# Performance work log

Hardware: AMD Instinct MI355X
Metric: run time of the kernel (lower is better)

Reference implementation:

```python
import jax, jax.numpy as jnp
import numpy as np

B, T, D = 64, 512, 512
H, DH = 8, 64  # head_num, att_embedding_size; H*DH == D
NEG = jnp.float32(-2.0**32 + 1)


def _pos_encoding(t, d):
    # Position_Embedding (mode='sum'): [cos, sin] concat over d/2 frequencies
    inv_freq = 1.0 / jnp.power(10000.0, 2.0 * jnp.arange(d // 2, dtype=jnp.float32) / d)
    pij = jnp.arange(t, dtype=jnp.float32)[:, None] * inv_freq[None, :]  # (T, d/2)
    return jnp.concatenate([jnp.cos(pij), jnp.sin(pij)], axis=-1)  # (T, d)


def setup_inputs() -> dict:
    key = jax.random.key(0)
    ks = jax.random.split(key, 9)
    queries = jax.random.normal(ks[0], (B, T, D), dtype=jnp.float32)
    keys = jax.random.normal(ks[1], (B, T, D), dtype=jnp.float32)
    query_lens = jax.random.randint(ks[2], (B, 1), 1, T + 1)
    key_lens = jax.random.randint(ks[3], (B, 1), 1, T + 1)
    W_Q = jax.random.truncated_normal(ks[4], -2., 2., (D, H * DH), dtype=jnp.float32) * 0.05
    W_K = jax.random.truncated_normal(ks[5], -2., 2., (D, H * DH), dtype=jnp.float32) * 0.05
    W_V = jax.random.truncated_normal(ks[6], -2., 2., (D, H * DH), dtype=jnp.float32) * 0.05
    fw1 = jax.random.normal(ks[7], (H * DH, 4 * H * DH), dtype=jnp.float32) * 0.02
    fw2 = jax.random.normal(ks[8], (4 * H * DH, H * DH), dtype=jnp.float32) * 0.02
    return {"queries": queries, "keys": keys, "query_lens": query_lens,
            "key_lens": key_lens, "W_Q": W_Q, "W_K": W_K, "W_V": W_V,
            "fw1": fw1, "fw2": fw2}


def reference(queries, keys, query_lens, key_lens, W_Q, W_K, W_V, fw1, fw2):
    # sequence masks (B, T) from lengths (B, 1)
    ar = jnp.arange(T)
    q_mask = (ar[None, :] < query_lens).astype(jnp.float32)  # (B, T)
    k_mask = ar[None, :] < key_lens                          # (B, T) bool

    pe = _pos_encoding(T, D)[None]  # (1, T, D)
    q_in = queries + pe
    k_in = keys + pe

    qp = jnp.einsum('btd,de->bte', q_in, W_Q).reshape(B, T, H, DH)
    kp = jnp.einsum('btd,de->bte', k_in, W_K)
    # DeepCTR quirk: values projected from the already-projected keys
    vp = jnp.einsum('btd,de->bte', kp, W_V).reshape(B, T, H, DH)
    kp = kp.reshape(B, T, H, DH)

    scores = jnp.einsum('bthd,bshd->bhts', qp, kp) / jnp.sqrt(jnp.float32(DH))
    scores = jnp.where(k_mask[:, None, None, :], scores, NEG)
    scores = scores - jnp.max(scores, axis=-1, keepdims=True)
    attn = jax.nn.softmax(scores, axis=-1)
    attn = attn * q_mask[:, None, :, None]

    out = jnp.einsum('bhts,bshd->bthd', attn, vp).reshape(B, T, H * DH)
    result = out + q_in  # residual uses PE-augmented queries

    ff = jnp.einsum('btd,df->btf', jax.nn.relu(jnp.einsum('btd,df->btf', result, fw1)), fw2)
    result = result + ff

    return jnp.mean(result, axis=1, keepdims=True)  # (B, 1, D)
```

## Files before the change

kernel.cpp:

```cpp
#include <hip/hip_runtime.h>

typedef unsigned short u16;
typedef __attribute__((ext_vector_type(8))) short short8;
typedef __attribute__((ext_vector_type(4))) float floatx4;

#define QSCALE 0.1803368801111204f

__device__ __forceinline__ u16 f2bf(float x) {
  union { float f; unsigned u; } un; un.f = x;
  unsigned r = un.u + 0x7fffu + ((un.u >> 16) & 1u);
  return (u16)(r >> 16);
}
__device__ __forceinline__ float bf2f(u16 h) {
  union { unsigned u; float f; } un; un.u = ((unsigned)h) << 16;
  return un.f;
}
__device__ __forceinline__ void gld16(const u16* g, u16* l) {
  __builtin_amdgcn_global_load_lds((__attribute__((address_space(1))) void*)g,
                                   (__attribute__((address_space(3))) void*)l, 16, 0, 0);
}

__global__ __launch_bounds__(256) void wtrans_all(const float* __restrict__ W_Q,
                                                  const float* __restrict__ W_K,
                                                  const float* __restrict__ fw1,
                                                  u16* __restrict__ WqT, u16* __restrict__ WkT,
                                                  u16* __restrict__ F1T) {
  __shared__ float tile[32][33];
  int L = blockIdx.x;
  const float* in;
  u16* out;
  int N, bx, by;
  if (L < 256) { in = W_Q; out = WqT; N = 512; bx = L & 15; by = L >> 4; }
  else if (L < 512) { L -= 256; in = W_K; out = WkT; N = 512; bx = L & 15; by = L >> 4; }
  else { L -= 512; in = fw1; out = F1T; N = 2048; bx = L & 63; by = L >> 6; }
  int tx = threadIdx.x, ty = threadIdx.y;
  int n0 = bx * 32, k0 = by * 32;
#pragma unroll
  for (int i = 0; i < 4; i++) {
    int kk = ty + i * 8;
    tile[kk][tx] = in[(size_t)(k0 + kk) * N + n0 + tx];
  }
  __syncthreads();
#pragma unroll
  for (int i = 0; i < 4; i++) {
    int nn = ty + i * 8;
    out[(size_t)(n0 + nn) * 512 + k0 + tx] = f2bf(tile[tx][nn]);
  }
}

__global__ __launch_bounds__(256) void wkv_kernel(const float* __restrict__ WK,
                                                  const float* __restrict__ WV,
                                                  u16* __restrict__ WkvT) {
  __shared__ float Kt[32][36];
  __shared__ float Vt[32][36];
  int nt = blockIdx.x & 15, dt = blockIdx.x >> 4;
  int n0 = nt * 32, d0 = dt * 32;
  int tid = threadIdx.x;
  int flat = tid * 4;
  int i4 = flat >> 5, j4 = flat & 31;
  int tn = tid & 15, td = tid >> 4;
  float acc00 = 0.f, acc01 = 0.f, acc10 = 0.f, acc11 = 0.f;
  for (int e0 = 0; e0 < 512; e0 += 32) {
    __syncthreads();
    *(float4*)&Kt[i4][j4] = *(const float4*)&WK[(size_t)(d0 + i4) * 512 + e0 + j4];
    *(float4*)&Vt[i4][j4] = *(const float4*)&WV[(size_t)(e0 + i4) * 512 + n0 + j4];
    __syncthreads();
#pragma unroll 8
    for (int e = 0; e < 32; e++) {
      float k0v = Kt[td * 2][e], k1v = Kt[td * 2 + 1][e];
      float v0 = Vt[e][tn * 2], v1 = Vt[e][tn * 2 + 1];
      acc00 += k0v * v0; acc01 += k0v * v1;
      acc10 += k1v * v0; acc11 += k1v * v1;
    }
  }
  size_t o = (size_t)(n0 + tn * 2) * 512 + d0 + td * 2;
  WkvT[o] = f2bf(acc00);
  WkvT[o + 1] = f2bf(acc10);
  WkvT[o + 512] = f2bf(acc01);
  WkvT[o + 513] = f2bf(acc11);
}

__global__ __launch_bounds__(256) void pe_add_kernel(const float* __restrict__ q,
                                                     const float* __restrict__ k,
                                                     u16* __restrict__ qb, u16* __restrict__ kb) {
  size_t flat = ((size_t)blockIdx.x * 256 + threadIdx.x) * 4;
  int d0 = (int)(flat & 511);
  int t = (int)((flat >> 9) & 511);
  const float4 qv = *(const float4*)(q + flat);
  const float4 kv = *(const float4*)(k + flat);
  float pe[4];
#pragma unroll
  for (int i = 0; i < 4; i++) {
    int d = d0 + i;
    int j = (d < 256) ? d : d - 256;
    float f = exp2f((float)j * -0.05190512648f);
    float arg = (float)t * f;
    pe[i] = (d < 256) ? cosf(arg) : sinf(arg);
  }
  u16 qo[4], ko[4];
  qo[0] = f2bf(qv.x + pe[0]); qo[1] = f2bf(qv.y + pe[1]);
  qo[2] = f2bf(qv.z + pe[2]); qo[3] = f2bf(qv.w + pe[3]);
  ko[0] = f2bf(kv.x + pe[0]); ko[1] = f2bf(kv.y + pe[1]);
  ko[2] = f2bf(kv.z + pe[2]); ko[3] = f2bf(kv.w + pe[3]);
  *(uint2*)(qb + flat) = *(const uint2*)qo;
  *(uint2*)(kb + flat) = *(const uint2*)ko;
}

template <int EPI, int MODE>
__global__ __launch_bounds__(256) void gemm_bt(const u16* __restrict__ A, const u16* __restrict__ Bt,
                                               u16* __restrict__ C, int NX, int KS, int N, int K,
                                               float* __restrict__ outp,
                                               const u16* __restrict__ A2, const u16* __restrict__ Bt2,
                                               u16* __restrict__ C2,
                                               const u16* __restrict__ A3, const u16* __restrict__ Bt3,
                                               u16* __restrict__ C3) {
  __shared__ u16 pool[16640];
  u16* Alds = pool;
  u16* Blds = pool + 8192;
  const int tid = threadIdx.x;
  const int lane = tid & 63, w = tid >> 6;
  const int quad = lane >> 4, cl = lane & 15;
  const int wm = w >> 1, wn = w & 1;
  int L = blockIdx.x;
  int seg = 0;
  if (MODE == 2) {
    int third = gridDim.x / 3;
    seg = L / third;
    L -= seg * third;
    if (seg == 1) { A = A2; Bt = Bt2; C = C2; }
    else if (seg == 2) { A = A3; Bt = Bt3; C = C3; }
  }
  const int xcd = L & 7, s = L >> 3;
  const int nx = s % NX;
  const int t2 = s / NX;
  const int ksl = t2 % KS;
  const int rgrp = t2 / KS;
  const int tm = (rgrp * 8 + xcd) * 128;
  const int tn = nx * 128;
  const int kbase = ksl * (K / KS);
  floatx4 acc[4][4] = {};
  const int nk = (K / KS) >> 6;
  const int srow = lane >> 3;
  const int sg = (lane & 7) ^ srow;
  for (int ks = 0; ks < nk; ks++) {
    __syncthreads();
    const int k0 = kbase + (ks << 6);
#pragma unroll
    for (int i = 0; i < 4; i++) {
      int c = w * 4 + i;
      int row = c * 8 + srow;
      gld16(A + ((size_t)(tm + row) * K + k0 + sg * 8), &Alds[c * 512]);
      gld16(Bt + ((size_t)(tn + row) * K + k0 + sg * 8), &Blds[c * 512]);
    }
    __syncthreads();
#pragma unroll
    for (int kh = 0; kh < 2; kh++) {
      short8 af[4], bfr[4];
      const int ga = (((kh << 2) + quad) ^ (cl & 7)) * 8;
#pragma unroll
      for (int f = 0; f < 4; f++) {
        af[f] = *(const short8*)&Alds[(wm * 64 + f * 16 + cl) * 64 + ga];
        bfr[f] = *(const short8*)&Blds[(wn * 64 + f * 16 + cl) * 64 + ga];
      }
#pragma unroll
      for (int fm = 0; fm < 4; fm++)
#pragma unroll
        for (int fn = 0; fn < 4; fn++)
          acc[fm][fn] = __builtin_amdgcn_mfma_f32_16x16x32_bf16(af[fm], bfr[fn], acc[fm][fn], 0, 0, 0);
    }
  }
  if constexpr (MODE == 2) {
    if (seg < 2) {
#pragma unroll
      for (int fm = 0; fm < 4; fm++)
#pragma unroll
        for (int fn = 0; fn < 4; fn++)
#pragma unroll
          for (int r = 0; r < 4; r++) {
            int row = tm + wm * 64 + fm * 16 + quad * 4 + r;
            int col = tn + wn * 64 + fn * 16 + cl;
            C[(size_t)row * N + col] = f2bf(acc[fm][fn][r]);
          }
    } else {
      __syncthreads();
      u16* Tr = pool;
#pragma unroll
      for (int fm = 0; fm < 4; fm++)
#pragma unroll
        for (int fn = 0; fn < 4; fn++)
#pragma unroll
          for (int r = 0; r < 4; r++) {
            int row = wm * 64 + fm * 16 + quad * 4 + r;
            int col = wn * 64 + fn * 16 + cl;
            Tr[col * 130 + row] = f2bf(acc[fm][fn][r]);
          }
      __syncthreads();
      int col = tid >> 1, half = tid & 1;
      int b = tm >> 9, gcol = tn + col;
      int h = gcol >> 6, d = gcol & 63;
      int s0 = (tm & 511) + half * 64;
      u16* dst = C + ((size_t)((b * 8 + h) * 64 + d) * 512 + s0);
      const u16* src = &Tr[col * 130 + half * 64];
#pragma unroll
      for (int j = 0; j < 8; j++) *(short8*)(dst + j * 8) = *(const short8*)(src + j * 8);
    }
  } else if constexpr (EPI == 0) {
#pragma unroll
    for (int fm = 0; fm < 4; fm++)
#pragma unroll
      for (int fn = 0; fn < 4; fn++)
#pragma unroll
        for (int r = 0; r < 4; r++) {
          int row = tm + wm * 64 + fm * 16 + quad * 4 + r;
          int col = tn + wn * 64 + fn * 16 + cl;
          C[(size_t)row * N + col] = f2bf(acc[fm][fn][r]);
        }
  }
}

__global__ __launch_bounds__(512, 2) void ffn1_256(const u16* __restrict__ A,
                                                   const u16* __restrict__ Bt,
                                                   float* __restrict__ outp) {
  __shared__ u16 lds[65536];
  const int K = 512;
  const int tid = threadIdx.x;
  const int lane = tid & 63, w = tid >> 6;
  const int quad = lane >> 4, cl = lane & 15;
  const int wm = w >> 2, wn = w & 3;
  int L = blockIdx.x;
  const int xcd = L & 7, s = L >> 3;
  const int nx = s & 7;
  const int rgrp = s >> 3;
  const int tm = (rgrp * 8 + xcd) * 256;
  const int tn = nx * 256;
  const int srow = lane >> 3;
  const int sg = (lane & 7) ^ srow;
  const int cb = w * 4;

  floatx4 acc[8][4] = {};

  {
    u16* Ab = lds;
    u16* Bb = lds + 16384;
#pragma unroll
    for (int i = 0; i < 4; i++) {
      int cc = cb + i, row = cc * 8 + srow;
      gld16(A + ((size_t)(tm + row) * K + sg * 8), &Ab[cc * 512]);
    }
#pragma unroll
    for (int i = 0; i < 4; i++) {
      int cc = cb + i, row = cc * 8 + srow;
      gld16(Bt + ((size_t)(tn + row) * K + sg * 8), &Bb[cc * 512]);
    }
  }

  const int nk = K >> 6;
#pragma unroll 1
  for (int kt = 0; kt < nk; kt++) {
    u16* Ab = lds + (kt & 1) * 32768;
    u16* Bb = Ab + 16384;
    u16* An = lds + ((kt & 1) ^ 1) * 32768;
    u16* Bn = An + 16384;
    const bool pf = (kt + 1 < nk);
    const int k0n = (kt + 1) << 6;
    if (pf) {
#pragma unroll
      for (int i = 0; i < 4; i++) {
        int cc = cb + i, row = cc * 8 + srow;
        gld16(A + ((size_t)(tm + row) * K + k0n + sg * 8), &An[cc * 512]);
      }
      asm volatile("s_waitcnt vmcnt(4)" ::: "memory");
    } else {
      asm volatile("s_waitcnt vmcnt(0)" ::: "memory");
    }
    __builtin_amdgcn_s_barrier();
    short8 a0[4][2], b0[2][2];
#pragma unroll
    for (int f = 0; f < 4; f++)
#pragma unroll
      for (int kh = 0; kh < 2; kh++)
        a0[f][kh] = *(const short8*)&Ab[(wm * 128 + f * 16 + cl) * 64 + ((((kh << 2) + quad)) ^ (cl & 7)) * 8];
#pragma unroll
    for (int n = 0; n < 2; n++)
#pragma unroll
      for (int kh = 0; kh < 2; kh++)
        b0[n][kh] = *(const short8*)&Bb[(wn * 64 + n * 16 + cl) * 64 + ((((kh << 2) + quad)) ^ (cl & 7)) * 8];
    __builtin_amdgcn_s_setprio(1);
#pragma unroll
    for (int f = 0; f < 4; f++)
#pragma unroll
      for (int n = 0; n < 2; n++)
#pragma unroll
        for (int kh = 0; kh < 2; kh++)
          acc[f][n] = __builtin_amdgcn_mfma_f32_16x16x32_bf16(a0[f][kh], b0[n][kh], acc[f][n], 0, 0, 0);
    __builtin_amdgcn_s_setprio(0);
    __builtin_amdgcn_s_barrier();
    if (pf) {
#pragma unroll
      for (int i = 0; i < 4; i++) {
        int cc = cb + i, row = cc * 8 + srow;
        gld16(Bt + ((size_t)(tn + row) * K + k0n + sg * 8), &Bn[cc * 512]);
      }
    }
    short8 b1[2][2];
#pragma unroll
    for (int n = 0; n < 2; n++)
#pragma unroll
      for (int kh = 0; kh < 2; kh++)
        b1[n][kh] = *(const short8*)&Bb[(wn * 64 + (n + 2) * 16 + cl) * 64 + ((((kh << 2) + quad)) ^ (cl & 7)) * 8];
    __builtin_amdgcn_s_setprio(1);
#pragma unroll
    for (int f = 0; f < 4; f++)
#pragma unroll
      for (int n = 0; n < 2; n++)
#pragma unroll
        for (int kh = 0; kh < 2; kh++)
          acc[f][n + 2] = __builtin_amdgcn_mfma_f32_16x16x32_bf16(a0[f][kh], b1[n][kh], acc[f][n + 2], 0, 0, 0);
    __builtin_amdgcn_s_setprio(0);
    __builtin_amdgcn_s_barrier();
    short8 a1[4][2];
#pragma unroll
    for (int f = 0; f < 4; f++)
#pragma unroll
      for (int kh = 0; kh < 2; kh++)
        a1[f][kh] = *(const short8*)&Ab[(wm * 128 + (f + 4) * 16 + cl) * 64 + ((((kh << 2) + quad)) ^ (cl & 7)) * 8];
    __builtin_amdgcn_s_setprio(1);
#pragma unroll
    for (int f = 0; f < 4; f++)
#pragma unroll
      for (int n = 0; n < 2; n++)
#pragma unroll
        for (int kh = 0; kh < 2; kh++)
          acc[f + 4][n + 2] = __builtin_amdgcn_mfma_f32_16x16x32_bf16(a1[f][kh], b1[n][kh], acc[f + 4][n + 2], 0, 0, 0);
    __builtin_amdgcn_s_setprio(0);
    __builtin_amdgcn_s_barrier();
    __builtin_amdgcn_s_setprio(1);
#pragma unroll
    for (int f = 0; f < 4; f++)
#pragma unroll
      for (int n = 0; n < 2; n++)
#pragma unroll
        for (int kh = 0; kh < 2; kh++)
          acc[f + 4][n] = __builtin_amdgcn_mfma_f32_16x16x32_bf16(a1[f][kh], b0[n][kh], acc[f + 4][n], 0, 0, 0);
    __builtin_amdgcn_s_setprio(0);
    __builtin_amdgcn_s_barrier();
  }

  float cs[4] = {0.f, 0.f, 0.f, 0.f};
#pragma unroll
  for (int f = 0; f < 8; f++)
#pragma unroll
    for (int n = 0; n < 4; n++)
#pragma unroll
      for (int r = 0; r < 4; r++) cs[n] += fmaxf(acc[f][n][r], 0.0f);
#pragma unroll
  for (int n = 0; n < 4; n++) {
    cs[n] += __shfl_xor(cs[n], 16);
    cs[n] += __shfl_xor(cs[n], 32);
  }
  if (quad == 0) {
    int b = tm >> 9;
#pragma unroll
    for (int n = 0; n < 4; n++)
      atomicAdd(outp + (size_t)b * 2048 + tn + wn * 64 + n * 16 + cl, cs[n]);
  }
}

__global__ __launch_bounds__(256) void ffn2_mean_kernel(const float* __restrict__ sums,
                                                        const float* __restrict__ fw2,
                                                        float* __restrict__ outp) {
  __shared__ float s[128];
  int fs = blockIdx.x & 15, b = blockIdx.x >> 4;
  int tid = threadIdx.x;
  if (tid < 128) s[tid] = sums[(size_t)b * 2048 + fs * 128 + tid];
  __syncthreads();
  const float* w = fw2 + (size_t)(fs * 128) * 512;
  float a0 = 0.f, a1 = 0.f;
#pragma unroll 4
  for (int f = 0; f < 128; f++) {
    float sv = s[f];
    a0 += sv * w[(size_t)f * 512 + tid];
    a1 += sv * w[(size_t)f * 512 + 256 + tid];
  }
  atomicAdd(outp + b * 512 + tid, a0 * (1.0f / 512.0f));
  atomicAdd(outp + b * 512 + 256 + tid, a1 * (1.0f / 512.0f));
}

__global__ __launch_bounds__(256) void attn_kernel(const u16* __restrict__ qp, const u16* __restrict__ kp,
                                                   const u16* __restrict__ vT, const u16* __restrict__ qin,
                                                   u16* __restrict__ resout, const int* __restrict__ qlen,
                                                   const int* __restrict__ klen, float* __restrict__ outp) {
  __shared__ u16 KPu[8704];
  __shared__ u16 Vlds[64 * 128];
  __shared__ float Csum[4][64];
  int L = blockIdx.x;
  int xcd = L & 7;
  int idx = L >> 3;
  int qt = idx & 7;
  int g = xcd + (idx >> 3) * 8;
  int h = g & 7, b = g >> 3;
  int tid = threadIdx.x, lane = tid & 63, w = tid >> 6;
  int quad = lane >> 4, cl = lane & 15;
  int kl = klen[b], ql = qlen[b];
  int q0 = qt * 64 + w * 16;

  if (qt * 64 >= ql) {
    int c = tid & 63, r0 = (tid >> 6) * 16;
    float sv = 0.f;
#pragma unroll
    for (int i = 0; i < 16; i++) {
      size_t idx2 = ((size_t)(b * 512 + qt * 64 + r0 + i) * 512) + h * 64 + c;
      u16 val = qin[idx2];
      resout[idx2] = val;
      sv += bf2f(val);
    }
    Csum[w][c] = sv;
    __syncthreads();
    if (tid < 64) {
      float t = Csum[0][tid] + Csum[1][tid] + Csum[2][tid] + Csum[3][tid];
      atomicAdd(outp + b * 512 + h * 64 + tid, t * (1.0f / 512.0f));
    }
    return;
  }
  bool wactive = q0 < ql;

  short8 qfrag[2];
#pragma unroll
  for (int ks = 0; ks < 2; ks++)
    qfrag[ks] = *(const short8*)(qp + ((size_t)(b * 512 + q0 + cl) * 512 + h * 64 + ks * 32 + quad * 8));
  const short8 ones8 = {(short)0x3F80, (short)0x3F80, (short)0x3F80, (short)0x3F80,
                        (short)0x3F80, (short)0x3F80, (short)0x3F80, (short)0x3F80};
  float m_r[4];
  floatx4 o[4] = {};
  floatx4 lacc = {};
#pragma unroll
  for (int r = 0; r < 4; r++) m_r[r] = -3.0e38f;

  int nkt = (kl + 127) >> 7;
  for (int kt = 0; kt < nkt; kt++) {
    __syncthreads();
#pragma unroll
    for (int i = 0; i < 4; i++) {
      int c = w * 4 + i;
      int row = c * 8 + (lane >> 3);
      int gc = (lane & 7) ^ (row & 7);
      gld16(kp + ((size_t)(b * 512 + kt * 128 + row) * 512 + h * 64 + gc * 8), &KPu[c * 512]);
    }
#pragma unroll
    for (int i = 0; i < 4; i++) {
      int c = w * 4 + i;
      int row = c * 4 + (lane >> 4);
      int gc = (lane & 15) ^ (row & 7);
      gld16(vT + ((size_t)((b * 8 + h) * 64 + row) * 512 + kt * 128 + gc * 8), &Vlds[c * 512]);
    }
    asm volatile("s_waitcnt vmcnt(4)" ::: "memory");
    __builtin_amdgcn_s_barrier();
    __builtin_amdgcn_sched_barrier(0);
    floatx4 sacc[8] = {};
    float mnew[4], alpha[4];
    if (wactive) {
      __builtin_amdgcn_s_setprio(1);
#pragma unroll
      for (int f = 0; f < 8; f++) {
        int krow = f * 16 + cl;
#pragma unroll
        for (int ks = 0; ks < 2; ks++) {
          int kc = ks * 4 + quad;
          short8 kf = *(const short8*)&KPu[krow * 64 + ((kc ^ (cl & 7)) * 8)];
          sacc[f] = __builtin_amdgcn_mfma_f32_16x16x32_bf16(qfrag[ks], kf, sacc[f], 0, 0, 0);
        }
      }
      __builtin_amdgcn_s_setprio(0);
#pragma unroll
      for (int r = 0; r < 4; r++) mnew[r] = m_r[r];
#pragma unroll
      for (int f = 0; f < 8; f++) {
        int key = kt * 128 + f * 16 + cl;
        bool ok = key < kl;
#pragma unroll
        for (int r = 0; r < 4; r++) {
          float v = ok ? sacc[f][r] * QSCALE : -4294967296.0f;
          sacc[f][r] = v;
          mnew[r] = fmaxf(mnew[r], v);
        }
      }
#pragma unroll
      for (int mk = 1; mk <= 8; mk <<= 1)
#pragma unroll
        for (int r = 0; r < 4; r++) mnew[r] = fmaxf(mnew[r], __shfl_xor(mnew[r], mk));
#pragma unroll
      for (int r = 0; r < 4; r++) {
        alpha[r] = exp2f(m_r[r] - mnew[r]);
        m_r[r] = mnew[r];
      }
    }
    __syncthreads();
    if (wactive) {
      u16* P = &KPu[w * 2176];
#pragma unroll
      for (int f = 0; f < 8; f++)
#pragma unroll
        for (int r = 0; r < 4; r++) {
          float p = exp2f(sacc[f][r] - mnew[r]);
          P[(quad * 4 + r) * 136 + f * 16 + cl] = f2bf(p);
        }
#pragma unroll
      for (int r = 0; r < 4; r++) lacc[r] *= alpha[r];
#pragma unroll
      for (int fd = 0; fd < 4; fd++)
#pragma unroll
        for (int r = 0; r < 4; r++) o[fd][r] *= alpha[r];
      __builtin_amdgcn_s_setprio(1);
#pragma unroll
      for (int k2 = 0; k2 < 4; k2++) {
        short8 pf = *(const short8*)&P[cl * 136 + k2 * 32 + quad * 8];
        lacc = __builtin_amdgcn_mfma_f32_16x16x32_bf16(pf, ones8, lacc, 0, 0, 0);
#pragma unroll
        for (int fd = 0; fd < 4; fd++) {
          int vrow = fd * 16 + cl;
          int sc = k2 * 4 + quad;
          short8 vf = *(const short8*)&Vlds[vrow * 128 + ((sc ^ (cl & 7)) * 8)];
          o[fd] = __builtin_amdgcn_mfma_f32_16x16x32_bf16(pf, vf, o[fd], 0, 0, 0);
        }
      }
      __builtin_amdgcn_s_setprio(0);
    }
  }
  float colsum[4] = {0.f, 0.f, 0.f, 0.f};
#pragma unroll
  for (int fd = 0; fd < 4; fd++)
#pragma unroll
    for (int r = 0; r < 4; r++) {
      int q = q0 + quad * 4 + r;
      float v = o[fd][r] / lacc[r];
      if (q >= ql) v = 0.f;
      size_t idx2 = (size_t)(b * 512 + q) * 512 + h * 64 + fd * 16 + cl;
      v += bf2f(qin[idx2]);
      resout[idx2] = f2bf(v);
      colsum[fd] += v;
    }
#pragma unroll
  for (int fd = 0; fd < 4; fd++) {
    colsum[fd] += __shfl_xor(colsum[fd], 16);
    colsum[fd] += __shfl_xor(colsum[fd], 32);
  }
  if (quad == 0) {
#pragma unroll
    for (int fd = 0; fd < 4; fd++) Csum[w][fd * 16 + cl] = colsum[fd];
  }
  __syncthreads();
  if (tid < 64) {
    float t = Csum[0][tid] + Csum[1][tid] + Csum[2][tid] + Csum[3][tid];
    atomicAdd(outp + b * 512 + h * 64 + tid, t * (1.0f / 512.0f));
  }
}

extern "C" void kernel_launch(void* const* d_in, const int* in_sizes, int n_in,
                              void* d_out, int out_size, void* d_ws, size_t ws_size,
                              hipStream_t stream) {
  const float* queries = (const float*)d_in[0];
  const float* keys = (const float*)d_in[1];
  const int* qlen = (const int*)d_in[2];
  const int* klen = (const int*)d_in[3];
  const float* W_Q = (const float*)d_in[4];
  const float* W_K = (const float*)d_in[5];
  const float* W_V = (const float*)d_in[6];
  const float* fw1 = (const float*)d_in[7];
  const float* fw2 = (const float*)d_in[8];
  float* outp = (float*)d_out;
  char* ws = (char*)d_ws;

  constexpr size_t SZ_W = 512 * 512 * 2;
  constexpr size_t SZ_F = 2048 * 512 * 2;
  constexpr size_t SZ_S = 64 * 2048 * 4;
  constexpr size_t SZ_T = (size_t)64 * 512 * 512 * 2;
  size_t o_WqT = 0;
  size_t o_WkT = o_WqT + SZ_W;
  size_t o_Wkv = o_WkT + SZ_W;
  size_t o_F1T = o_Wkv + SZ_W;
  size_t o_SUM = o_F1T + SZ_F;
  size_t o_ABCD = o_SUM + SZ_S;
  size_t o_E = o_ABCD + 4 * SZ_T;
  size_t NEED = o_E + SZ_T;
  if (ws_size < NEED) return;

  u16* WqT = (u16*)(ws + o_WqT);
  u16* WkT = (u16*)(ws + o_WkT);
  u16* WkvT = (u16*)(ws + o_Wkv);
  u16* F1T = (u16*)(ws + o_F1T);
  float* sums = (float*)(ws + o_SUM);
  u16* q_in = (u16*)(ws + o_ABCD);
  u16* k_in = (u16*)(ws + o_ABCD + SZ_T);
  u16* qp = (u16*)(ws + o_ABCD + 2 * SZ_T);
  u16* kpb = (u16*)(ws + o_ABCD + 3 * SZ_T);
  u16* vT = (u16*)(ws + o_E);
  u16* resb = k_in;

  hipMemsetAsync(d_out, 0, (size_t)out_size * sizeof(float), stream);
  hipMemsetAsync(sums, 0, SZ_S, stream);

  wtrans_all<<<1536, dim3(32, 8), 0, stream>>>(W_Q, W_K, fw1, WqT, WkT, F1T);
  wkv_kernel<<<256, 256, 0, stream>>>(W_K, W_V, WkvT);
  pe_add_kernel<<<16384, 256, 0, stream>>>(queries, keys, q_in, k_in);

  gemm_bt<0, 2><<<3 * 1024, 256, 0, stream>>>(q_in, WqT, qp, 4, 1, 512, 512, nullptr,
                                              k_in, WkT, kpb, k_in, WkvT, vT);

  attn_kernel<<<4096, 256, 0, stream>>>(qp, kpb, vT, q_in, resb, qlen, klen, outp);

  ffn1_256<<<1024, 512, 0, stream>>>(resb, F1T, sums);
  ffn2_mean_kernel<<<1024, 256, 0, stream>>>(sums, fw2, outp);
}
```

Baseline: 404.6 us.

## Use 256x256 double-buffered projection GEMM and precompute positional encoding table

Measured after the change: 397.9 us. About the same (-1.7%).

```diff
diff --git a/kernel.cpp b/kernel.cpp
--- a/kernel.cpp
+++ b/kernel.cpp
@@ -80,14 +80,10 @@
   WkvT[o + 513] = f2bf(acc11);
 }
 
-__global__ __launch_bounds__(256) void pe_add_kernel(const float* __restrict__ q,
-                                                     const float* __restrict__ k,
-                                                     u16* __restrict__ qb, u16* __restrict__ kb) {
-  size_t flat = ((size_t)blockIdx.x * 256 + threadIdx.x) * 4;
-  int d0 = (int)(flat & 511);
-  int t = (int)((flat >> 9) & 511);
-  const float4 qv = *(const float4*)(q + flat);
-  const float4 kv = *(const float4*)(k + flat);
+__global__ __launch_bounds__(256) void pe_table_kernel(float* __restrict__ pet) {
+  int flat = (blockIdx.x * 256 + threadIdx.x) * 4;
+  int d0 = flat & 511;
+  int t = flat >> 9;
   float pe[4];
 #pragma unroll
   for (int i = 0; i < 4; i++) {
@@ -97,124 +93,202 @@
     float arg = (float)t * f;
     pe[i] = (d < 256) ? cosf(arg) : sinf(arg);
   }
+  *(float4*)(pet + flat) = *(const float4*)pe;
+}
+
+__global__ __launch_bounds__(256) void pe_add_kernel(const float* __restrict__ q,
+                                                     const float* __restrict__ k,
+                                                     const float* __restrict__ pet,
+                                                     u16* __restrict__ qb, u16* __restrict__ kb) {
+  size_t flat = ((size_t)blockIdx.x * 256 + threadIdx.x) * 4;
+  const float4 qv = *(const float4*)(q + flat);
+  const float4 kv = *(const float4*)(k + flat);
+  const float4 pv = *(const float4*)(pet + (flat & 262143));
   u16 qo[4], ko[4];
-  qo[0] = f2bf(qv.x + pe[0]); qo[1] = f2bf(qv.y + pe[1]);
-  qo[2] = f2bf(qv.z + pe[2]); qo[3] = f2bf(qv.w + pe[3]);
-  ko[0] = f2bf(kv.x + pe[0]); ko[1] = f2bf(kv.y + pe[1]);
-  ko[2] = f2bf(kv.z + pe[2]); ko[3] = f2bf(kv.w + pe[3]);
+  qo[0] = f2bf(qv.x + pv.x); qo[1] = f2bf(qv.y + pv.y);
+  qo[2] = f2bf(qv.z + pv.z); qo[3] = f2bf(qv.w + pv.w);
+  ko[0] = f2bf(kv.x + pv.x); ko[1] = f2bf(kv.y + pv.y);
+  ko[2] = f2bf(kv.z + pv.z); ko[3] = f2bf(kv.w + pv.w);
   *(uint2*)(qb + flat) = *(const uint2*)qo;
   *(uint2*)(kb + flat) = *(const uint2*)ko;
 }
 
-template <int EPI, int MODE>
-__global__ __launch_bounds__(256) void gemm_bt(const u16* __restrict__ A, const u16* __restrict__ Bt,
-                                               u16* __restrict__ C, int NX, int KS, int N, int K,
-                                               float* __restrict__ outp,
-                                               const u16* __restrict__ A2, const u16* __restrict__ Bt2,
-                                               u16* __restrict__ C2,
-                                               const u16* __restrict__ A3, const u16* __restrict__ Bt3,
-                                               u16* __restrict__ C3) {
-  __shared__ u16 pool[16640];
-  u16* Alds = pool;
-  u16* Blds = pool + 8192;
+__global__ __launch_bounds__(512, 2) void proj_256(const u16* __restrict__ q_in,
+                                                   const u16* __restrict__ k_in,
+                                                   const u16* __restrict__ WqT,
+                                                   const u16* __restrict__ WkT,
+                                                   const u16* __restrict__ WkvT,
+                                                   u16* __restrict__ qp,
+                                                   u16* __restrict__ kpb,
+                                                   u16* __restrict__ vTp) {
+  __shared__ u16 lds[65536];
+  const int K = 512;
   const int tid = threadIdx.x;
   const int lane = tid & 63, w = tid >> 6;
   const int quad = lane >> 4, cl = lane & 15;
-  const int wm = w >> 1, wn = w & 1;
+  const int wm = w >> 2, wn = w & 3;
   int L = blockIdx.x;
-  int seg = 0;
-  if (MODE == 2) {
-    int third = gridDim.x / 3;
-    seg = L / third;
-    L -= seg * third;
-    if (seg == 1) { A = A2; Bt = Bt2; C = C2; }
-    else if (seg == 2) { A = A3; Bt = Bt3; C = C3; }
-  }
+  const int seg = L >> 8;
+  L &= 255;
+  const u16* A = (seg == 0) ? q_in : k_in;
+  const u16* Bt = (seg == 0) ? WqT : (seg == 1) ? WkT : WkvT;
   const int xcd = L & 7, s = L >> 3;
-  const int nx = s % NX;
-  const int t2 = s / NX;
-  const int ksl = t2 % KS;
-  const int rgrp = t2 / KS;
-  const int tm = (rgrp * 8 + xcd) * 128;
-  const int tn = nx * 128;
-  const int kbase = ksl * (K / KS);
-  floatx4 acc[4][4] = {};
-  const int nk = (K / KS) >> 6;
+  const int nx = s & 1;
+  const int rgrp = s >> 1;
+  const int tm = (rgrp * 8 + xcd) * 256;
+  const int tn = nx * 256;
   const int srow = lane >> 3;
   const int sg = (lane & 7) ^ srow;
-  for (int ks = 0; ks < nk; ks++) {
-    __syncthreads();
-    const int k0 = kbase + (ks << 6);
+  const int cb = w * 4;
+
+  floatx4 acc[8][4] = {};
+
+  {
+    u16* Ab = lds;
+    u16* Bb = lds + 16384;
 #pragma unroll
     for (int i = 0; i < 4; i++) {
-      int c = w * 4 + i;
-      int row = c * 8 + srow;
-      gld16(A + ((size_t)(tm + row) * K + k0 + sg * 8), &Alds[c * 512]);
-      gld16(Bt + ((size_t)(tn + row) * K + k0 + sg * 8), &Blds[c * 512]);
-    }
-    __syncthreads();
-#pragma unroll
-    for (int kh = 0; kh < 2; kh++) {
-      short8 af[4], bfr[4];
-      const int ga = (((kh << 2) + quad) ^ (cl & 7)) * 8;
-#pragma unroll
-      for (int f = 0; f < 4; f++) {
-        af[f] = *(const short8*)&Alds[(wm * 64 + f * 16 + cl) * 64 + ga];
-        bfr[f] = *(const short8*)&Blds[(wn * 64 + f * 16 + cl) * 64 + ga];
-      }
-#pragma unroll
-      for (int fm = 0; fm < 4; fm++)
-#pragma unroll
-        for (int fn = 0; fn < 4; fn++)
-          acc[fm][fn] = __builtin_amdgcn_mfma_f32_16x16x32_bf16(af[fm], bfr[fn], acc[fm][fn], 0, 0, 0);
-    }
-  }
-  if constexpr (MODE == 2) {
-    if (seg < 2) {
-#pragma unroll
-      for (int fm = 0; fm < 4; fm++)
-#pragma unroll
-        for (int fn = 0; fn < 4; fn++)
-#pragma unroll
-          for (int r = 0; r < 4; r++) {
-            int row = tm + wm * 64 + fm * 16 + quad * 4 + r;
-            int col = tn + wn * 64 + fn * 16 + cl;
-            C[(size_t)row * N + col] = f2bf(acc[fm][fn][r]);
-          }
+      int cc = cb + i, row = cc * 8 + srow;
+      gld16(A + ((size_t)(tm + row) * K + sg * 8), &Ab[cc * 512]);
+    }
+#pragma unroll
+    for (int i = 0; i < 4; i++) {
+      int cc = cb + i, row = cc * 8 + srow;
+      gld16(Bt + ((size_t)(tn + row) * K + sg * 8), &Bb[cc * 512]);
+    }
+  }
+
+  const int nk = K >> 6;
+#pragma unroll 1
+  for (int kt = 0; kt < nk; kt++) {
+    u16* Ab = lds + (kt & 1) * 32768;
+    u16* Bb = Ab + 16384;
+    u16* An = lds + ((kt & 1) ^ 1) * 32768;
+    u16* Bn = An + 16384;
+    const bool pf = (kt + 1 < nk);
+    const int k0n = (kt + 1) << 6;
+    if (pf) {
+#pragma unroll
+      for (int i = 0; i < 4; i++) {
+        int cc = cb + i, row = cc * 8 + srow;
+        gld16(A + ((size_t)(tm + row) * K + k0n + sg * 8), &An[cc * 512]);
+      }
+#pragma unroll
+      for (int i = 0; i < 4; i++) {
+        int cc = cb + i, row = cc * 8 + srow;
+        gld16(Bt + ((size_t)(tn + row) * K + k0n + sg * 8), &Bn[cc * 512]);
+      }
+      asm volatile("s_waitcnt vmcnt(8)" ::: "memory");
     } else {
+      asm volatile("s_waitcnt vmcnt(0)" ::: "memory");
+    }
+    __builtin_amdgcn_s_barrier();
+    short8 a0[4][2], b0[2][2];
+#pragma unroll
+    for (int f = 0; f < 4; f++)
+#pragma unroll
+      for (int kh = 0; kh < 2; kh++)
+        a0[f][kh] = *(const short8*)&Ab[(wm * 128 + f * 16 + cl) * 64 + ((((kh << 2) + quad)) ^ (cl & 7)) * 8];
+#pragma unroll
+    for (int n = 0; n < 2; n++)
+#pragma unroll
+      for (int kh = 0; kh < 2; kh++)
+        b0[n][kh] = *(const short8*)&Bb[(wn * 64 + n * 16 + cl) * 64 + ((((kh << 2) + quad)) ^ (cl & 7)) * 8];
+    __builtin_amdgcn_s_setprio(1);
+#pragma unroll
+    for (int f = 0; f < 4; f++)
+#pragma unroll
+      for (int n = 0; n < 2; n++)
+#pragma unroll
+        for (int kh = 0; kh < 2; kh++)
+          acc[f][n] = __builtin_amdgcn_mfma_f32_16x16x32_bf16(a0[f][kh], b0[n][kh], acc[f][n], 0, 0, 0);
+    __builtin_amdgcn_s_setprio(0);
+    __builtin_amdgcn_s_barrier();
+    short8 b1[2][2];
+#pragma unroll
+    for (int n = 0; n < 2; n++)
+#pragma unroll
+      for (int kh = 0; kh < 2; kh++)
+        b1[n][kh] = *(const short8*)&Bb[(wn * 64 + (n + 2) * 16 + cl) * 64 + ((((kh << 2) + quad)) ^ (cl & 7)) * 8];
+    __builtin_amdgcn_s_setprio(1);
+#pragma unroll
+    for (int f = 0; f < 4; f++)
+#pragma unroll
+      for (int n = 0; n < 2; n++)
+#pragma unroll
+        for (int kh = 0; kh < 2; kh++)
+          acc[f][n + 2] = __builtin_amdgcn_mfma_f32_16x16x32_bf16(a0[f][kh], b1[n][kh], acc[f][n + 2], 0, 0, 0);
+    __builtin_amdgcn_s_setprio(0);
+    __builtin_amdgcn_s_barrier();
+    short8 a1[4][2];
+#pragma unroll
+    for (int f = 0; f < 4; f++)
+#pragma unroll
+      for (int kh = 0; kh < 2; kh++)
+        a1[f][kh] = *(const short8*)&Ab[(wm * 128 + (f + 4) * 16 + cl) * 64 + ((((kh << 2) + quad)) ^ (cl & 7)) * 8];
+    __builtin_amdgcn_s_setprio(1);
+#pragma unroll
+    for (int f = 0; f < 4; f++)
+#pragma unroll
+      for (int n = 0; n < 2; n++)
+#pragma unroll
+        for (int kh = 0; kh < 2; kh++)
+          acc[f + 4][n + 2] = __builtin_amdgcn_mfma_f32_16x16x32_bf16(a1[f][kh], b1[n][kh], acc[f + 4][n + 2], 0, 0, 0);
+    __builtin_amdgcn_s_setprio(0);
+    __builtin_amdgcn_s_barrier();
+    __builtin_amdgcn_s_setprio(1);
+#pragma unroll
+    for (int f = 0; f < 4; f++)
+#pragma unroll
+      for (int n = 0; n < 2; n++)
+#pragma unroll
+        for (int kh = 0; kh < 2; kh++)
+          acc[f + 4][n] = __builtin_amdgcn_mfma_f32_16x16x32_bf16(a1[f][kh], b0[n][kh], acc[f + 4][n], 0, 0, 0);
+    __builtin_amdgcn_s_setprio(0);
+    __builtin_amdgcn_s_barrier();
+  }
+
+  if (seg < 2) {
+    u16* C = (seg == 0) ? qp : kpb;
+#pragma unroll
+    for (int f = 0; f < 8; f++)
+#pragma unroll
+      for (int n = 0; n < 4; n++)
+#pragma unroll
+        for (int r = 0; r < 4; r++) {
+          int row = tm + wm * 128 + f * 16 + quad * 4 + r;
+          int col = tn + wn * 64 + n * 16 + cl;
+          C[(size_t)row * 512 + col] = f2bf(acc[f][n][r]);
+        }
+  } else {
+    const int b = tm >> 9, sbase = tm & 511;
+#pragma unroll 1
+    for (int p = 0; p < 2; p++) {
       __syncthreads();
-      u16* Tr = pool;
-#pragma unroll
-      for (int fm = 0; fm < 4; fm++)
-#pragma unroll
-        for (int fn = 0; fn < 4; fn++)
-#pragma unroll
-          for (int r = 0; r < 4; r++) {
-            int row = wm * 64 + fm * 16 + quad * 4 + r;
-            int col = wn * 64 + fn * 16 + cl;
-            Tr[col * 130 + row] = f2bf(acc[fm][fn][r]);
-          }
+      if ((wn >> 1) == p) {
+        int cbase = (wn & 1) * 64;
+#pragma unroll
+        for (int f = 0; f < 8; f++)
+#pragma unroll
+          for (int n = 0; n < 4; n++)
+#pragma unroll
+            for (int r = 0; r < 4; r++) {
+              int tc = cbase + n * 16 + cl;
+              int row = wm * 128 + f * 16 + quad * 4 + r;
+              lds[tc * 264 + row] = f2bf(acc[f][n][r]);
+            }
+      }
       __syncthreads();
-      int col = tid >> 1, half = tid & 1;
-      int b = tm >> 9, gcol = tn + col;
-      int h = gcol >> 6, d = gcol & 63;
-      int s0 = (tm & 511) + half * 64;
-      u16* dst = C + ((size_t)((b * 8 + h) * 64 + d) * 512 + s0);
-      const u16* src = &Tr[col * 130 + half * 64];
-#pragma unroll
-      for (int j = 0; j < 8; j++) *(short8*)(dst + j * 8) = *(const short8*)(src + j * 8);
-    }
-  } else if constexpr (EPI == 0) {
-#pragma unroll
-    for (int fm = 0; fm < 4; fm++)
-#pragma unroll
-      for (int fn = 0; fn < 4; fn++)
-#pragma unroll
-        for (int r = 0; r < 4; r++) {
-          int row = tm + wm * 64 + fm * 16 + quad * 4 + r;
-          int col = tn + wn * 64 + fn * 16 + cl;
-          C[(size_t)row * N + col] = f2bf(acc[fm][fn][r]);
-        }
+      int col = tid >> 2;
+      int e = tn + p * 128 + col;
+      int h = e >> 6, d = e & 63;
+      u16* dst = vTp + ((size_t)((b * 8 + h) * 64 + d) * 512 + sbase);
+#pragma unroll
+      for (int j = 0; j < 8; j++) {
+        int chunk = (tid & 3) + j * 4;
+        *(short8*)(dst + chunk * 8) = *(const short8*)&lds[col * 264 + chunk * 8];
+      }
+    }
   }
 }
 
@@ -269,39 +343,37 @@
         int cc = cb + i, row = cc * 8 + srow;
         gld16(A + ((size_t)(tm + row) * K + k0n + sg * 8), &An[cc * 512]);
       }
-      asm volatile("s_waitcnt vmcnt(4)" ::: "memory");
-    } else {
-      asm volatile("s_waitcnt vmcnt(0)" ::: "memory");
-    }
-    __builtin_amdgcn_s_barrier();
-    short8 a0[4][2], b0[2][2];
-#pragma unroll
-    for (int f = 0; f < 4; f++)
-#pragma unroll
-      for (int kh = 0; kh < 2; kh++)
-        a0[f][kh] = *(const short8*)&Ab[(wm * 128 + f * 16 + cl) * 64 + ((((kh << 2) + quad)) ^ (cl & 7)) * 8];
-#pragma unroll
-    for (int n = 0; n < 2; n++)
-#pragma unroll
-      for (int kh = 0; kh < 2; kh++)
-        b0[n][kh] = *(const short8*)&Bb[(wn * 64 + n * 16 + cl) * 64 + ((((kh << 2) + quad)) ^ (cl & 7)) * 8];
-    __builtin_amdgcn_s_setprio(1);
-#pragma unroll
-    for (int f = 0; f < 4; f++)
-#pragma unroll
-      for (int n = 0; n < 2; n++)
-#pragma unroll
-        for (int kh = 0; kh < 2; kh++)
-          acc[f][n] = __builtin_amdgcn_mfma_f32_16x16x32_bf16(a0[f][kh], b0[n][kh], acc[f][n], 0, 0, 0);
-    __builtin_amdgcn_s_setprio(0);
-    __builtin_amdgcn_s_barrier();
-    if (pf) {
 #pragma unroll
       for (int i = 0; i < 4; i++) {
         int cc = cb + i, row = cc * 8 + srow;
         gld16(Bt + ((size_t)(tn + row) * K + k0n + sg * 8), &Bn[cc * 512]);
       }
-    }
+      asm volatile("s_waitcnt vmcnt(8)" ::: "memory");
+    } else {
+      asm volatile("s_waitcnt vmcnt(0)" ::: "memory");
+    }
+    __builtin_amdgcn_s_barrier();
+    short8 a0[4][2], b0[2][2];
+#pragma unroll
+    for (int f = 0; f < 4; f++)
+#pragma unroll
+      for (int kh = 0; kh < 2; kh++)
+        a0[f][kh] = *(const short8*)&Ab[(wm * 128 + f * 16 + cl) * 64 + ((((kh << 2) + quad)) ^ (cl & 7)) * 8];
+#pragma unroll
+    for (int n = 0; n < 2; n++)
+#pragma unroll
+      for (int kh = 0; kh < 2; kh++)
+        b0[n][kh] = *(const short8*)&Bb[(wn * 64 + n * 16 + cl) * 64 + ((((kh << 2) + quad)) ^ (cl & 7)) * 8];
+    __builtin_amdgcn_s_setprio(1);
+#pragma unroll
+    for (int f = 0; f < 4; f++)
+#pragma unroll
+      for (int n = 0; n < 2; n++)
+#pragma unroll
+        for (int kh = 0; kh < 2; kh++)
+          acc[f][n] = __builtin_amdgcn_mfma_f32_16x16x32_bf16(a0[f][kh], b0[n][kh], acc[f][n], 0, 0, 0);
+    __builtin_amdgcn_s_setprio(0);
+    __builtin_amdgcn_s_barrier();
     short8 b1[2][2];
 #pragma unroll
     for (int n = 0; n < 2; n++)
@@ -594,6 +666,7 @@
   u16* qp = (u16*)(ws + o_ABCD + 2 * SZ_T);
   u16* kpb = (u16*)(ws + o_ABCD + 3 * SZ_T);
   u16* vT = (u16*)(ws + o_E);
+  float* pet = (float*)(ws + o_E);
   u16* resb = k_in;
 
   hipMemsetAsync(d_out, 0, (size_t)out_size * sizeof(float), stream);
@@ -601,10 +674,10 @@
 
   wtrans_all<<<1536, dim3(32, 8), 0, stream>>>(W_Q, W_K, fw1, WqT, WkT, F1T);
   wkv_kernel<<<256, 256, 0, stream>>>(W_K, W_V, WkvT);
-  pe_add_kernel<<<16384, 256, 0, stream>>>(queries, keys, q_in, k_in);
-
-  gemm_bt<0, 2><<<3 * 1024, 256, 0, stream>>>(q_in, WqT, qp, 4, 1, 512, 512, nullptr,
-                                              k_in, WkT, kpb, k_in, WkvT, vT);
+  pe_table_kernel<<<256, 256, 0, stream>>>(pet);
+  pe_add_kernel<<<16384, 256, 0, stream>>>(queries, keys, pet, q_in, k_in);
+
+  proj_256<<<768, 512, 0, stream>>>(q_in, k_in, WqT, WkT, WkvT, qp, kpb, vT);
 
   attn_kernel<<<4096, 256, 0, stream>>>(qp, kpb, vT, q_in, resb, qlen, klen, outp);
 
```
